# Optimization experiments

Measured on AMD Instinct MI355X. Metric: run time of the kernel, lower is better.

Reference implementation:

```python
import jax, jax.numpy as jnp
import numpy as np

EPS = 1e-5
GROUPS = 8


def setup_inputs() -> dict:
    key = jax.random.key(0)
    ks = jax.random.split(key, 3)
    b, c, h, w = 8, 256, 64, 64
    x = jax.random.normal(ks[0], (b, c, h, w), dtype=jnp.float32)
    # 1x1 convs are just channel matmuls; store weights as [out_ch, in_ch]
    qkv_w = jax.random.normal(ks[1], (3 * c, c), dtype=jnp.float32) * (c ** -0.5)
    qkv_b = jnp.zeros((3 * c,), dtype=jnp.float32)
    out_w = jax.random.normal(ks[2], (c, c), dtype=jnp.float32) * (c ** -0.5)
    out_b = jnp.zeros((c,), dtype=jnp.float32)
    gn_w = jnp.ones((c,), dtype=jnp.float32)
    gn_b = jnp.zeros((c,), dtype=jnp.float32)
    return {"x": x, "gn_w": gn_w, "gn_b": gn_b, "qkv_w": qkv_w,
            "qkv_b": qkv_b, "out_w": out_w, "out_b": out_b}


def _group_norm(x, gn_w, gn_b):
    # x: [b, c, h, w]; normalize per (group, sample) over (c//g, h, w)
    b, c, h, w = x.shape
    xg = x.reshape(b, GROUPS, c // GROUPS, h * w)
    mean = xg.mean(axis=(2, 3), keepdims=True)
    var = xg.var(axis=(2, 3), keepdims=True)
    xn = (xg - mean) * jax.lax.rsqrt(var + EPS)
    xn = xn.reshape(b, c, h * w)
    return xn * gn_w[None, :, None] + gn_b[None, :, None]


def reference(x, gn_w, gn_b, qkv_w, qkv_b, out_w, out_b):
    b, c, h, w = x.shape
    scale = 1.0 / np.sqrt(c).astype(np.float32)  # matches channels ** -0.5
    nx = _group_norm(x, gn_w, gn_b)                       # [b, c, n]
    qkv = jnp.einsum('oc,bcn->bon', qkv_w, nx) + qkv_b[None, :, None]
    q, k, v = qkv[:, :c], qkv[:, c:2 * c], qkv[:, 2 * c:]  # each [b, c, n]
    attn = jnp.einsum('bci,bcj->bij', q, k) * scale        # [b, n, n]
    attn = jax.nn.softmax(attn, axis=-1)
    out = jnp.einsum('bij,bcj->bci', attn, v)              # [b, c, n]
    out = jnp.einsum('oc,bcn->bon', out_w, out) + out_b[None, :, None]
    return out.reshape(b, c, h, w) + x
```

## Files before the change

kernel.cpp:

```cpp
#include <hip/hip_runtime.h>
#include <math.h>


#define Bn 8
#define Cn 256
#define HWn 4096
#define Gn 8
#define CPGn 32
#define Mqkv 768
#define EPSf 1e-5f
#define QSCALEf 0.0625f
#define RTHR 8.0f

typedef short bf16x8 __attribute__((ext_vector_type(8)));
typedef float f32x4 __attribute__((ext_vector_type(4)));
typedef float f32x16 __attribute__((ext_vector_type(16)));

__device__ __forceinline__ unsigned short f2bf(float f) {
  union { float f; unsigned u; } v; v.f = f;
  unsigned r = v.u + 0x7FFFu + ((v.u >> 16) & 1u);
  return (unsigned short)(r >> 16);
}

__device__ __forceinline__ int cvt_pk_bf16(float lo, float hi) {
  int d;
  asm("v_cvt_pk_bf16_f32 %0, %1, %2" : "=v"(d) : "v"(lo), "v"(hi));
  return d;
}

__global__ __launch_bounds__(1024)
void gn_stats_kernel(const float* __restrict__ x, const float* __restrict__ gn_w,
                     const float* __restrict__ gn_b, float* __restrict__ s_out,
                     float* __restrict__ t_out) {
  const int b = blockIdx.x / Gn, g = blockIdx.x % Gn;
  const float4* base = (const float4*)(x + ((size_t)(b * Cn + g * CPGn)) * HWn);
  const int n4 = CPGn * HWn / 4;
  float sum = 0.f, sq = 0.f;
  for (int i = threadIdx.x; i < n4; i += 1024) {
    float4 v = base[i];
    sum += (v.x + v.y) + (v.z + v.w);
    sq  += (v.x * v.x + v.y * v.y) + (v.z * v.z + v.w * v.w);
  }
  __shared__ float ss[1024], s2[1024];
  ss[threadIdx.x] = sum; s2[threadIdx.x] = sq;
  __syncthreads();
  for (int off = 512; off > 0; off >>= 1) {
    if ((int)threadIdx.x < off) {
      ss[threadIdx.x] += ss[threadIdx.x + off];
      s2[threadIdx.x] += s2[threadIdx.x + off];
    }
    __syncthreads();
  }
  if (threadIdx.x < CPGn) {
    const float inv_n = 1.f / (float)(CPGn * HWn);
    float mean = ss[0] * inv_n;
    float var  = s2[0] * inv_n - mean * mean;
    float rstd = rsqrtf(var + EPSf);
    int c = g * CPGn + (int)threadIdx.x;
    float sc = gn_w[c] * rstd;
    s_out[b * Cn + c] = sc;
    t_out[b * Cn + c] = gn_b[c] - mean * sc;
  }
}

__global__ __launch_bounds__(256)
void affine_transpose_kernel(const float* __restrict__ x, const float* __restrict__ s_aff,
                             const float* __restrict__ t_aff, unsigned short* __restrict__ nxT) {
  const int bid = blockIdx.x;
  const int b = bid & 7, r = bid >> 3;
  const int c0 = (r & 3) * 64, n0 = (r >> 2) * 64;
  const int tid = threadIdx.x;
  __shared__ unsigned int ld32[64][33];
  const float* xb = x + ((size_t)(b * Cn + c0)) * HWn + n0;
  const int cl0 = tid >> 4, nn = (tid & 15) * 4;
#pragma unroll
  for (int it = 0; it < 4; ++it) {
    int cl = cl0 + 16 * it;
    int c = c0 + cl;
    float sc = s_aff[b * Cn + c], sh = t_aff[b * Cn + c];
    float4 v = *(const float4*)(xb + (size_t)cl * HWn + nn);
    ld32[cl][(nn >> 1) + 0] = (unsigned)cvt_pk_bf16(v.x * sc + sh, v.y * sc + sh);
    ld32[cl][(nn >> 1) + 1] = (unsigned)cvt_pk_bf16(v.z * sc + sh, v.w * sc + sh);
  }
  __syncthreads();
#pragma unroll
  for (int it = 0; it < 2; ++it) {
    int chunk = tid + 256 * it;
    int n = chunk >> 3, cg = chunk & 7;
    union { unsigned short u[8]; bf16x8 v; } o;
#pragma unroll
    for (int k = 0; k < 8; ++k) {
      unsigned w32 = ld32[cg * 8 + k][n >> 1];
      o.u[k] = (unsigned short)((n & 1) ? (w32 >> 16) : (w32 & 0xffffu));
    }
    *(bf16x8*)(nxT + ((size_t)(b * HWn + n0 + n)) * Cn + c0 + cg * 8) = o.v;
  }
}

__global__ __launch_bounds__(256, 2)
void qkv_gemm_kernel(const unsigned short* __restrict__ nxT, const float* __restrict__ w,
                     const float* __restrict__ wb, unsigned short* __restrict__ Qt,
                     unsigned short* __restrict__ Kt, unsigned short* __restrict__ Vb) {
  const int bid = blockIdx.x;
  const int b = bid & 7, r = bid >> 3;
  const int n0 = (r & 63) * 64, m0 = (r >> 6) * 128;
  const int tid = threadIdx.x;
  const int wv = tid >> 6, l = tid & 63;
  const int l15 = l & 15, lq = l >> 4;
  const int ob = m0 + wv * 32;

  bf16x8 wf[2][8];
#pragma unroll
  for (int g = 0; g < 2; ++g) {
    const float* wr = w + (size_t)(ob + g * 16 + l15) * Cn + lq * 8;
#pragma unroll
    for (int kc = 0; kc < 8; ++kc) {
      float4 a = *(const float4*)(wr + kc * 32);
      float4 c4 = *(const float4*)(wr + kc * 32 + 4);
      union { int w4[4]; bf16x8 v; } u;
      u.w4[0] = cvt_pk_bf16(a.x, a.y);  u.w4[1] = cvt_pk_bf16(a.z, a.w);
      u.w4[2] = cvt_pk_bf16(c4.x, c4.y); u.w4[3] = cvt_pk_bf16(c4.z, c4.w);
      wf[g][kc] = u.v;
    }
  }

  const unsigned short* nb = nxT + (size_t)b * HWn * Cn + lq * 8;
  f32x4 acc[2][4];
#pragma unroll
  for (int g = 0; g < 2; ++g)
#pragma unroll
    for (int s = 0; s < 4; ++s) acc[g][s] = (f32x4)(0.f);

  const bool isV = (m0 >= 512);
#pragma unroll
  for (int s = 0; s < 4; ++s) {
    const unsigned short* np = nb + (size_t)(n0 + s * 16 + l15) * Cn;
#pragma unroll
    for (int kc = 0; kc < 8; ++kc) {
      bf16x8 xf = *(const bf16x8*)(np + kc * 32);
      if (!isV) {
        acc[0][s] = __builtin_amdgcn_mfma_f32_16x16x32_bf16(wf[0][kc], xf, acc[0][s], 0, 0, 0);
        acc[1][s] = __builtin_amdgcn_mfma_f32_16x16x32_bf16(wf[1][kc], xf, acc[1][s], 0, 0, 0);
      } else {
        acc[0][s] = __builtin_amdgcn_mfma_f32_16x16x32_bf16(xf, wf[0][kc], acc[0][s], 0, 0, 0);
        acc[1][s] = __builtin_amdgcn_mfma_f32_16x16x32_bf16(xf, wf[1][kc], acc[1][s], 0, 0, 0);
      }
    }
  }

  if (!isV) {
    unsigned short* dst = (m0 < 256) ? Qt : Kt;
    const float scl = (m0 < 256) ? QSCALEf : 1.0f;
#pragma unroll
    for (int g = 0; g < 2; ++g) {
      int cb = ((ob + g * 16) & 255) + lq * 4;
      float b0 = wb[ob + g * 16 + lq * 4 + 0];
      float b1 = wb[ob + g * 16 + lq * 4 + 1];
      float b2 = wb[ob + g * 16 + lq * 4 + 2];
      float b3 = wb[ob + g * 16 + lq * 4 + 3];
#pragma unroll
      for (int s = 0; s < 4; ++s) {
        int n = n0 + s * 16 + l15;
        ushort4 pk;
        pk.x = f2bf((acc[g][s][0] + b0) * scl);
        pk.y = f2bf((acc[g][s][1] + b1) * scl);
        pk.z = f2bf((acc[g][s][2] + b2) * scl);
        pk.w = f2bf((acc[g][s][3] + b3) * scl);
        *(ushort4*)(dst + ((size_t)(b * HWn + n)) * Cn + cb) = pk;
      }
    }
  } else {
#pragma unroll
    for (int g = 0; g < 2; ++g) {
      int o = ob + g * 16 + l15;
      int c = o - 512;
      float bias = wb[o];
#pragma unroll
      for (int s = 0; s < 4; ++s) {
        int n = n0 + s * 16 + lq * 4;
        ushort4 pk;
        pk.x = f2bf(acc[g][s][0] + bias);
        pk.y = f2bf(acc[g][s][1] + bias);
        pk.z = f2bf(acc[g][s][2] + bias);
        pk.w = f2bf(acc[g][s][3] + bias);
        *(ushort4*)(Vb + ((size_t)(b * Cn + c)) * HWn + n) = pk;
      }
    }
  }
}

__global__ __launch_bounds__(256, 1)
void attn_kernel(const unsigned short* __restrict__ Qt,
                 const unsigned short* __restrict__ Kt,
                 const unsigned short* __restrict__ Vb,
                 unsigned short* __restrict__ outp) {
  const int bid = blockIdx.x;
  const int b = bid & 7, i0 = (bid >> 3) * 128;
  const int tid = threadIdx.x;
  const int wv = tid >> 6, l = tid & 63;
  const int l31 = l & 31, hi = l >> 5;

  __shared__ unsigned short Ks[8192];
  __shared__ unsigned short Vs[8192];
  char* KsB = (char*)Ks;
  char* VsB = (char*)Vs;

  const unsigned short* Qb = Qt + ((size_t)b * HWn + i0) * Cn;
  const unsigned short* Kb = Kt + (size_t)b * HWn * Cn;
  const unsigned short* Vg = Vb + (size_t)b * Cn * HWn;

  bf16x8 qf[16];
  {
    const unsigned short* qrow = Qb + (size_t)(wv * 32 + l31) * Cn + hi * 8;
#pragma unroll
    for (int kc = 0; kc < 16; ++kc) qf[kc] = *(const bf16x8*)(qrow + kc * 16);
  }

  const int kco = (((tid >> 6) << 1) | ((tid >> 5) & 1));
  const unsigned short* gK = Kb + (size_t)(tid & 31) * Cn + kco * 8;
  const int vc  = ((tid >> 7) << 5) | (tid & 31);
  const int vjo = ((tid >> 5) & 1) | (((tid >> 6) & 1) << 1);
  const unsigned short* gV = Vg + (size_t)vc * HWn + vjo * 8;

  bf16x8 kst[4], vst[4];
#pragma unroll
  for (int q = 0; q < 4; ++q) kst[q] = *(const bf16x8*)(gK + q * 64);
#pragma unroll
  for (int q = 0; q < 4; ++q) vst[q] = *(const bf16x8*)(gV + (size_t)q * 64 * HWn);
  gK += 32 * Cn; gV += 32;

  f32x16 oa[8];
#pragma unroll
  for (int cb = 0; cb < 8; ++cb) oa[cb] = (f32x16)(0.f);
  float m_i = -INFINITY, l_i = 0.f;

#pragma unroll 1
  for (int t = 0; t < 128; ++t) {
#pragma unroll
    for (int q = 0; q < 4; ++q) *(bf16x8*)(KsB + tid * 16 + q * 4096) = kst[q];
#pragma unroll
    for (int q = 0; q < 4; ++q) *(bf16x8*)(VsB + tid * 16 + q * 4096) = vst[q];
    __syncthreads();
    if (t < 127) {
#pragma unroll
      for (int q = 0; q < 4; ++q) kst[q] = *(const bf16x8*)(gK + q * 64);
#pragma unroll
      for (int q = 0; q < 4; ++q) vst[q] = *(const bf16x8*)(gV + (size_t)q * 64 * HWn);
      gK += 32 * Cn; gV += 32;
    }

    f32x16 sa = (f32x16)(0.f);
#pragma unroll
    for (int kc = 0; kc < 16; ++kc) {
      bf16x8 kf = *(const bf16x8*)(KsB + l * 16 + kc * 1024);
      sa = __builtin_amdgcn_mfma_f32_32x32x16_bf16(kf, qf[kc], sa, 0, 0, 0);
    }

    float p[16];
#pragma unroll
    for (int r = 0; r < 16; ++r) p[r] = sa[r];
    float rm = p[0];
#pragma unroll
    for (int r = 1; r < 16; ++r) rm = fmaxf(rm, p[r]);
    rm = fmaxf(rm, __shfl_xor(rm, 32));
    if (!__all(rm - m_i <= RTHR)) {
      float mn = fmaxf(m_i, rm);
      float alpha = __expf(m_i - mn);
      m_i = mn;
      l_i *= alpha;
#pragma unroll
      for (int cb = 0; cb < 8; ++cb)
#pragma unroll
        for (int r = 0; r < 16; ++r) oa[cb][r] *= alpha;
    }
    float rs = 0.f;
#pragma unroll
    for (int r = 0; r < 16; ++r) { p[r] = __expf(p[r] - m_i); rs += p[r]; }
    rs += __shfl_xor(rs, 32);
    l_i += rs;

    int d0 = cvt_pk_bf16(p[0],  p[1]),  d1 = cvt_pk_bf16(p[2],  p[3]);
    int d2 = cvt_pk_bf16(p[4],  p[5]),  d3 = cvt_pk_bf16(p[6],  p[7]);
    int d4 = cvt_pk_bf16(p[8],  p[9]),  d5 = cvt_pk_bf16(p[10], p[11]);
    int d6 = cvt_pk_bf16(p[12], p[13]), d7 = cvt_pk_bf16(p[14], p[15]);
    int x0 = __shfl_xor(d0, 32), x1 = __shfl_xor(d1, 32);
    int x2 = __shfl_xor(d2, 32), x3 = __shfl_xor(d3, 32);
    int x4 = __shfl_xor(d4, 32), x5 = __shfl_xor(d5, 32);
    int x6 = __shfl_xor(d6, 32), x7 = __shfl_xor(d7, 32);
    union { int w[4]; bf16x8 v; } pf0, pf1;
    pf0.w[0] = hi ? x2 : d0; pf0.w[1] = hi ? x3 : d1;
    pf0.w[2] = hi ? d2 : x0; pf0.w[3] = hi ? d3 : x1;
    pf1.w[0] = hi ? x6 : d4; pf1.w[1] = hi ? x7 : d5;
    pf1.w[2] = hi ? d6 : x4; pf1.w[3] = hi ? d7 : x5;

#pragma unroll
    for (int cb = 0; cb < 8; ++cb) {
      bf16x8 vf0 = *(const bf16x8*)(VsB + l * 16 + (2 * cb + 0) * 1024);
      bf16x8 vf1 = *(const bf16x8*)(VsB + l * 16 + (2 * cb + 1) * 1024);
      oa[cb] = __builtin_amdgcn_mfma_f32_32x32x16_bf16(vf0, pf0.v, oa[cb], 0, 0, 0);
      oa[cb] = __builtin_amdgcn_mfma_f32_32x32x16_bf16(vf1, pf1.v, oa[cb], 0, 0, 0);
    }
    __syncthreads();
  }

  float il = 1.f / l_i;
  unsigned short* ob = outp + ((size_t)b * HWn + (size_t)(i0 + wv * 32 + l31)) * Cn;
#pragma unroll
  for (int cb = 0; cb < 8; ++cb) {
#pragma unroll
    for (int g = 0; g < 4; ++g) {
      ushort4 s4;
      s4.x = f2bf(oa[cb][g * 4 + 0] * il);
      s4.y = f2bf(oa[cb][g * 4 + 1] * il);
      s4.z = f2bf(oa[cb][g * 4 + 2] * il);
      s4.w = f2bf(oa[cb][g * 4 + 3] * il);
      *(ushort4*)(ob + cb * 32 + 4 * hi + 8 * g) = s4;
    }
  }
}

__global__ __launch_bounds__(256, 2)
void out_gemm_kernel(const unsigned short* __restrict__ tmpT, const float* __restrict__ w,
                     const float* __restrict__ wb, const float* __restrict__ xres,
                     float* __restrict__ y) {
  const int bid = blockIdx.x;
  const int b = bid & 7, r = bid >> 3;
  const int n0 = (r & 63) * 64, m0 = (r >> 6) * 128;
  const int tid = threadIdx.x;
  const int wv = tid >> 6, l = tid & 63;
  const int l15 = l & 15, lq = l >> 4;
  const int ob = m0 + wv * 32;

  bf16x8 wf[2][8];
#pragma unroll
  for (int g = 0; g < 2; ++g) {
    const float* wr = w + (size_t)(ob + g * 16 + l15) * Cn + lq * 8;
#pragma unroll
    for (int kc = 0; kc < 8; ++kc) {
      float4 a = *(const float4*)(wr + kc * 32);
      float4 c4 = *(const float4*)(wr + kc * 32 + 4);
      union { int w4[4]; bf16x8 v; } u;
      u.w4[0] = cvt_pk_bf16(a.x, a.y);  u.w4[1] = cvt_pk_bf16(a.z, a.w);
      u.w4[2] = cvt_pk_bf16(c4.x, c4.y); u.w4[3] = cvt_pk_bf16(c4.z, c4.w);
      wf[g][kc] = u.v;
    }
  }

  const unsigned short* tb = tmpT + (size_t)b * HWn * Cn + lq * 8;
  f32x4 acc[2][4];
#pragma unroll
  for (int g = 0; g < 2; ++g)
#pragma unroll
    for (int s = 0; s < 4; ++s) acc[g][s] = (f32x4)(0.f);

#pragma unroll
  for (int s = 0; s < 4; ++s) {
    const unsigned short* tp = tb + (size_t)(n0 + s * 16 + l15) * Cn;
#pragma unroll
    for (int kc = 0; kc < 8; ++kc) {
      bf16x8 tf = *(const bf16x8*)(tp + kc * 32);
      acc[0][s] = __builtin_amdgcn_mfma_f32_16x16x32_bf16(tf, wf[0][kc], acc[0][s], 0, 0, 0);
      acc[1][s] = __builtin_amdgcn_mfma_f32_16x16x32_bf16(tf, wf[1][kc], acc[1][s], 0, 0, 0);
    }
  }

#pragma unroll
  for (int g = 0; g < 2; ++g) {
    int o = ob + g * 16 + l15;
    float bias = wb[o];
#pragma unroll
    for (int s = 0; s < 4; ++s) {
      int n = n0 + s * 16 + lq * 4;
      size_t idx = ((size_t)(b * Cn + o)) * HWn + n;
      float4 xr = *(const float4*)(xres + idx);
      float4 out;
      out.x = acc[g][s][0] + bias + xr.x;
      out.y = acc[g][s][1] + bias + xr.y;
      out.z = acc[g][s][2] + bias + xr.z;
      out.w = acc[g][s][3] + bias + xr.w;
      *(float4*)(y + idx) = out;
    }
  }
}

extern "C" void kernel_launch(void* const* d_in, const int* in_sizes, int n_in,
                              void* d_out, int out_size, void* d_ws, size_t ws_size,
                              hipStream_t stream) {
  (void)in_sizes; (void)n_in; (void)out_size; (void)ws_size;
  const float* x     = (const float*)d_in[0];
  const float* gn_w  = (const float*)d_in[1];
  const float* gn_b  = (const float*)d_in[2];
  const float* qkv_w = (const float*)d_in[3];
  const float* qkv_b = (const float*)d_in[4];
  const float* out_w = (const float*)d_in[5];
  const float* out_b = (const float*)d_in[6];
  float* out = (float*)d_out;

  char* ws = (char*)d_ws;
  float* s_aff = (float*)ws;
  float* t_aff = s_aff + Bn * Cn;
  unsigned short* Qt  = (unsigned short*)(ws + 16384);
  unsigned short* Kt  = Qt  + (size_t)Bn * HWn * Cn;
  unsigned short* Vb  = Kt  + (size_t)Bn * HWn * Cn;
  unsigned short* nxT = Vb  + (size_t)Bn * HWn * Cn;
  unsigned short* tmpT = nxT + (size_t)Bn * HWn * Cn;

  gn_stats_kernel<<<dim3(Bn * Gn), 1024, 0, stream>>>(x, gn_w, gn_b, s_aff, t_aff);
  affine_transpose_kernel<<<dim3(2048), 256, 0, stream>>>(x, s_aff, t_aff, nxT);
  qkv_gemm_kernel<<<dim3(3072), 256, 0, stream>>>(nxT, qkv_w, qkv_b, Qt, Kt, Vb);
  attn_kernel<<<dim3(256), 256, 0, stream>>>(Qt, Kt, Vb, tmpT);
  out_gemm_kernel<<<dim3(1024), 256, 0, stream>>>(tmpT, out_w, out_b, x, out);
}
```

Baseline: 394.1 us.

## Split attention key range in two and merge partials in a combine kernel

Result: slower. 410.1 us (+4.0%).

```diff
diff --git a/kernel.cpp b/kernel.cpp
--- a/kernel.cpp
+++ b/kernel.cpp
@@ -20,6 +20,11 @@
   union { float f; unsigned u; } v; v.f = f;
   unsigned r = v.u + 0x7FFFu + ((v.u >> 16) & 1u);
   return (unsigned short)(r >> 16);
+}
+
+__device__ __forceinline__ float bf2f(unsigned short u) {
+  union { unsigned u; float f; } v; v.u = ((unsigned)u) << 16;
+  return v.f;
 }
 
 __device__ __forceinline__ int cvt_pk_bf16(float lo, float hi) {
@@ -193,9 +198,9 @@
 void attn_kernel(const unsigned short* __restrict__ Qt,
                  const unsigned short* __restrict__ Kt,
                  const unsigned short* __restrict__ Vb,
-                 unsigned short* __restrict__ outp) {
+                 unsigned short* __restrict__ pO, float* __restrict__ pML) {
   const int bid = blockIdx.x;
-  const int b = bid & 7, i0 = (bid >> 3) * 128;
+  const int b = bid & 7, part = (bid >> 3) & 1, i0 = (bid >> 4) * 128;
   const int tid = threadIdx.x;
   const int wv = tid >> 6, l = tid & 63;
   const int l31 = l & 31, hi = l >> 5;
@@ -217,10 +222,10 @@
   }
 
   const int kco = (((tid >> 6) << 1) | ((tid >> 5) & 1));
-  const unsigned short* gK = Kb + (size_t)(tid & 31) * Cn + kco * 8;
+  const unsigned short* gK = Kb + (size_t)((tid & 31) + part * 2048) * Cn + kco * 8;
   const int vc  = ((tid >> 7) << 5) | (tid & 31);
   const int vjo = ((tid >> 5) & 1) | (((tid >> 6) & 1) << 1);
-  const unsigned short* gV = Vg + (size_t)vc * HWn + vjo * 8;
+  const unsigned short* gV = Vg + (size_t)vc * HWn + vjo * 8 + part * 2048;
 
   bf16x8 kst[4], vst[4];
 #pragma unroll
@@ -235,13 +240,13 @@
   float m_i = -INFINITY, l_i = 0.f;
 
 #pragma unroll 1
-  for (int t = 0; t < 128; ++t) {
+  for (int t = 0; t < 64; ++t) {
 #pragma unroll
     for (int q = 0; q < 4; ++q) *(bf16x8*)(KsB + tid * 16 + q * 4096) = kst[q];
 #pragma unroll
     for (int q = 0; q < 4; ++q) *(bf16x8*)(VsB + tid * 16 + q * 4096) = vst[q];
     __syncthreads();
-    if (t < 127) {
+    if (t < 63) {
 #pragma unroll
       for (int q = 0; q < 4; ++q) kst[q] = *(const bf16x8*)(gK + q * 64);
 #pragma unroll
@@ -303,24 +308,64 @@
     __syncthreads();
   }
 
-  float il = 1.f / l_i;
-  unsigned short* ob = outp + ((size_t)b * HWn + (size_t)(i0 + wv * 32 + l31)) * Cn;
+  unsigned short* pOb = pO + (size_t)bid * (128 * 256);
+  const int row = wv * 32 + l31;
 #pragma unroll
   for (int cb = 0; cb < 8; ++cb) {
 #pragma unroll
     for (int g = 0; g < 4; ++g) {
       ushort4 s4;
-      s4.x = f2bf(oa[cb][g * 4 + 0] * il);
-      s4.y = f2bf(oa[cb][g * 4 + 1] * il);
-      s4.z = f2bf(oa[cb][g * 4 + 2] * il);
-      s4.w = f2bf(oa[cb][g * 4 + 3] * il);
-      *(ushort4*)(ob + cb * 32 + 4 * hi + 8 * g) = s4;
-    }
+      s4.x = f2bf(oa[cb][g * 4 + 0]);
+      s4.y = f2bf(oa[cb][g * 4 + 1]);
+      s4.z = f2bf(oa[cb][g * 4 + 2]);
+      s4.w = f2bf(oa[cb][g * 4 + 3]);
+      *(ushort4*)(pOb + row * 256 + cb * 32 + 4 * hi + 8 * g) = s4;
+    }
+  }
+  if (hi == 0) {
+    pML[(size_t)bid * 256 + row * 2 + 0] = m_i;
+    pML[(size_t)bid * 256 + row * 2 + 1] = l_i;
+  }
+}
+
+__global__ __launch_bounds__(256)
+void attn_combine_kernel(unsigned short* __restrict__ pO, const float* __restrict__ pML) {
+  const int bid = blockIdx.x;
+  const int b = bid & 7, itile = bid >> 3;
+  const int tid = threadIdx.x;
+  const int p0 = b + itile * 16, p1 = p0 + 8;
+  unsigned short* B0 = pO + (size_t)p0 * (128 * 256);
+  const unsigned short* B1 = pO + (size_t)p1 * (128 * 256);
+
+  __shared__ float g0S[128], g1S[128];
+  if (tid < 128) {
+    float m0 = pML[(size_t)p0 * 256 + tid * 2], l0 = pML[(size_t)p0 * 256 + tid * 2 + 1];
+    float m1 = pML[(size_t)p1 * 256 + tid * 2], l1 = pML[(size_t)p1 * 256 + tid * 2 + 1];
+    float ms = fmaxf(m0, m1);
+    float w0 = __expf(m0 - ms), w1 = __expf(m1 - ms);
+    float id = 1.f / (w0 * l0 + w1 * l1);
+    g0S[tid] = w0 * id; g1S[tid] = w1 * id;
+  }
+  __syncthreads();
+
+#pragma unroll
+  for (int k = 0; k < 16; ++k) {
+    int chunk = tid + 256 * k;
+    int row = chunk >> 5, cc = (chunk & 31) * 8;
+    int off = row * 256 + cc;
+    float g0 = g0S[row], g1 = g1S[row];
+    union { unsigned short u[8]; bf16x8 v; } v0, v1, o;
+    v0.v = *(const bf16x8*)(B0 + off);
+    v1.v = *(const bf16x8*)(B1 + off);
+#pragma unroll
+    for (int e = 0; e < 8; ++e)
+      o.u[e] = f2bf(g0 * bf2f(v0.u[e]) + g1 * bf2f(v1.u[e]));
+    *(bf16x8*)(B0 + off) = o.v;
   }
 }
 
 __global__ __launch_bounds__(256, 2)
-void out_gemm_kernel(const unsigned short* __restrict__ tmpT, const float* __restrict__ w,
+void out_gemm_kernel(const unsigned short* __restrict__ pO, const float* __restrict__ w,
                      const float* __restrict__ wb, const float* __restrict__ xres,
                      float* __restrict__ y) {
   const int bid = blockIdx.x;
@@ -346,7 +391,8 @@
     }
   }
 
-  const unsigned short* tb = tmpT + (size_t)b * HWn * Cn + lq * 8;
+  const int slot = b + ((n0 >> 7) << 4);
+  const unsigned short* tb = pO + (size_t)slot * (128 * 256) + (size_t)(n0 & 127) * 256 + lq * 8;
   f32x4 acc[2][4];
 #pragma unroll
   for (int g = 0; g < 2; ++g)
@@ -355,7 +401,7 @@
 
 #pragma unroll
   for (int s = 0; s < 4; ++s) {
-    const unsigned short* tp = tb + (size_t)(n0 + s * 16 + l15) * Cn;
+    const unsigned short* tp = tb + (size_t)(s * 16 + l15) * 256;
 #pragma unroll
     for (int kc = 0; kc < 8; ++kc) {
       bf16x8 tf = *(const bf16x8*)(tp + kc * 32);
@@ -397,17 +443,20 @@
   float* out = (float*)d_out;
 
   char* ws = (char*)d_ws;
+  const size_t BHC = (size_t)Bn * HWn * Cn;
   float* s_aff = (float*)ws;
   float* t_aff = s_aff + Bn * Cn;
   unsigned short* Qt  = (unsigned short*)(ws + 16384);
-  unsigned short* Kt  = Qt  + (size_t)Bn * HWn * Cn;
-  unsigned short* Vb  = Kt  + (size_t)Bn * HWn * Cn;
-  unsigned short* nxT = Vb  + (size_t)Bn * HWn * Cn;
-  unsigned short* tmpT = nxT + (size_t)Bn * HWn * Cn;
+  unsigned short* Kt  = Qt + BHC;
+  unsigned short* Vb  = Kt + BHC;
+  unsigned short* nxT = Vb + BHC;
+  unsigned short* pO  = nxT;
+  float* pML = (float*)((char*)pO + (size_t)512 * 32768 * 2);
 
   gn_stats_kernel<<<dim3(Bn * Gn), 1024, 0, stream>>>(x, gn_w, gn_b, s_aff, t_aff);
   affine_transpose_kernel<<<dim3(2048), 256, 0, stream>>>(x, s_aff, t_aff, nxT);
   qkv_gemm_kernel<<<dim3(3072), 256, 0, stream>>>(nxT, qkv_w, qkv_b, Qt, Kt, Vb);
-  attn_kernel<<<dim3(256), 256, 0, stream>>>(Qt, Kt, Vb, tmpT);
-  out_gemm_kernel<<<dim3(1024), 256, 0, stream>>>(tmpT, out_w, out_b, x, out);
-}
+  attn_kernel<<<dim3(512), 256, 0, stream>>>(Qt, Kt, Vb, pO, pML);
+  attn_combine_kernel<<<dim3(256), 256, 0, stream>>>(pO, pML);
+  out_gemm_kernel<<<dim3(1024), 256, 0, stream>>>(pO, out_w, out_b, x, out);
+}
```
